# Optimization experiments

Measured on AMD Instinct MI355X. Metric: run time of the kernel, lower is better.

Reference implementation:

```python
import jax, jax.numpy as jnp
import numpy as np

# Production-scale dims
B, DZ, NW, NH, K = 8, 32, 48, 48, 25          # batch, dim_z, grid width/height, n_objects_max
W_RAW = H_RAW = 384.0                          # raw image size
SIZE_MIN, SIZE_MAX = 12.0, 48.0                # object size bounds
SCORE_T, OVER_T = 0.1, 0.3                     # score_threshold, overlap_threshold


def _conv1x1(x, w, b):
    # x: (B, d, nW, nH), w: (o, d), b: (o,) -> (B, o, nW, nH)  [Decoder1by1Linear]
    return jnp.einsum('bdwh,od->bowh', x, w) + b[None, :, None, None]


def _to_box_list(x):
    # (B, nW, nH) -> (N, B) with N = nW*nH, matching convert_to_box_list's permute(2,3,0,1).view
    return jnp.transpose(x, (1, 2, 0)).reshape(-1, x.shape[0])


def _nms(probT, x1, y1, x2, y2, k_max, score_t, over_t):
    # probT, x1..y2: (B, N). Greedy score/overlap NMS -> idx (B, K) int32, mask (B, N) float
    area = (x2 - x1) * (y2 - y1)
    xi1 = jnp.maximum(x1[:, :, None], x1[:, None, :])
    yi1 = jnp.maximum(y1[:, :, None], y1[:, None, :])
    xi2 = jnp.minimum(x2[:, :, None], x2[:, None, :])
    yi2 = jnp.minimum(y2[:, :, None], y2[:, None, :])
    inter = jnp.clip(xi2 - xi1, 0.0) * jnp.clip(yi2 - yi1, 0.0)
    union = area[:, :, None] + area[:, None, :] - inter
    iou = inter / jnp.maximum(union, 1e-8)                      # (B, N, N)
    possible0 = probT > score_t
    Bsz, N = probT.shape
    idx0 = jnp.zeros((Bsz, k_max), jnp.int32)
    val0 = jnp.zeros((Bsz, k_max), bool)

    def body(k, carry):
        possible, idxb, valb = carry
        masked = jnp.where(possible, probT, -jnp.inf)
        sel = jnp.argmax(masked, axis=1).astype(jnp.int32)      # (B,)
        ok = jnp.take_along_axis(possible, sel[:, None], axis=1)[:, 0]
        row = jnp.take_along_axis(iou, sel[:, None, None], axis=1)[:, 0, :]
        possible = possible & (row <= over_t)                   # suppresses sel itself (IoU=1)
        return possible, idxb.at[:, k].set(sel), valb.at[:, k].set(ok)

    _, idxb, valb = jax.lax.fori_loop(0, k_max, body, (possible0, idx0, val0))
    mask = jnp.zeros((Bsz, N), probT.dtype).at[jnp.arange(Bsz)[:, None], idxb].max(
        valb.astype(probT.dtype))
    return idxb, mask


def setup_inputs() -> dict:
    key = jax.random.key(0)
    ks = jax.random.split(key, 5)
    return {
        'zwhere_sample': jax.random.normal(ks[0], (B, DZ, NW, NH), jnp.float32),
        'w_zwhere': 0.2 * jax.random.normal(ks[1], (4, DZ), jnp.float32),
        'b_zwhere': jnp.zeros((4,), jnp.float32),
        'logit_sample': jax.random.normal(ks[2], (B, DZ, NW, NH), jnp.float32),
        'w_logit': 0.2 * jax.random.normal(ks[3], (1, DZ), jnp.float32),
        'b_logit': jnp.zeros((1,), jnp.float32),
        'weight_logits': jax.random.normal(ks[4], (K, B, 1, int(W_RAW), int(H_RAW)), jnp.float32),
    }


def reference(zwhere_sample, w_zwhere, b_zwhere, logit_sample, w_logit, b_logit, weight_logits):
    nW, nH = zwhere_sample.shape[-2:]
    # --- box decoding from zwhere latent map ---
    t = jax.nn.sigmoid(_conv1x1(zwhere_sample, w_zwhere, b_zwhere))  # (B,4,nW,nH)
    tx, ty, tw, th = t[:, 0], t[:, 1], t[:, 2], t[:, 3]
    ix = jnp.arange(nW, dtype=t.dtype)[:, None]   # ij meshgrid rows
    iy = jnp.arange(nH, dtype=t.dtype)[None, :]
    bx = W_RAW * (ix + tx) / nW
    by = H_RAW * (iy + ty) / nH
    bw = SIZE_MIN + (SIZE_MAX - SIZE_MIN) * tw
    bh = SIZE_MIN + (SIZE_MAX - SIZE_MIN) * th
    bx_l, by_l = _to_box_list(bx), _to_box_list(by)   # (N, B)
    bw_l, bh_l = _to_box_list(bw), _to_box_list(bh)
    # --- probability map from logit latent map ---
    p_map = jax.nn.sigmoid(_conv1x1(logit_sample, w_logit, b_logit))  # (B,1,nW,nH)
    prob_all = _to_box_list(p_map[:, 0])              # (N, B)
    probT = prob_all.T                                 # (B, N)
    x1 = (bx_l - 0.5 * bw_l).T
    x2 = (bx_l + 0.5 * bw_l).T
    y1 = (by_l - 0.5 * bh_l).T
    y2 = (by_l + 0.5 * bh_l).T
    # --- NMS under stop_gradient (torch.no_grad in original) ---
    sg = jax.lax.stop_gradient
    idxb, maskB = _nms(sg(probT), sg(x1), sg(y1), sg(x2), sg(y2), K, SCORE_T, OVER_T)
    # prob_few = gather(prob_all * nms_mask, index_top_k): differentiable w.r.t. prob_all
    prob_few = jnp.take_along_axis(probT * maskB, idxb, axis=1).T   # (K, B)
    # --- mask compositing (from_weights_to_masks over the object dim) ---
    big_weight = jax.nn.softplus(weight_logits)       # (K, B, 1, W, H)
    sum_w = jnp.sum(big_weight, axis=0, keepdims=True)
    big_mask = jnp.tanh(sum_w) * (big_weight / jnp.clip(sum_w, 1e-6))
    # probability-weighted masks (downstream compositing)
    return prob_few[:, :, None, None, None] * big_mask  # (K, B, 1, W, H)
```

## Files before the change

kernel.cpp:

```cpp
#include <hip/hip_runtime.h>
#include <math.h>

#define BATCH 8
#define DZ    32
#define NWH   48
#define NBOX  (NWH*NWH)
#define KMAX  25
#define PIX   (384*384)
#define NTOT  (BATCH*NBOX)
#define NW9   9

typedef float vfloat4 __attribute__((ext_vector_type(4)));

__device__ __forceinline__ float sigm(float x) { return 1.0f / (1.0f + expf(-x)); }
__device__ __forceinline__ float sp_fast(float x) {
    return fmaxf(x, 0.0f) + __logf(1.0f + __expf(-fabsf(x)));
}

__global__ __launch_bounds__(64) void conv_kernel(
    const float* __restrict__ z, const float* __restrict__ wz, const float* __restrict__ bz,
    const float* __restrict__ lg, const float* __restrict__ wl, const float* __restrict__ bl,
    float* __restrict__ ws)
{
    int t = blockIdx.x * 64 + threadIdx.x;
    int b = t / 576, j = t % 576;
    int iw = j / 12, ihq = j % 12;

    const float* zb = z  + (((size_t)b * DZ) * NWH + iw) * NWH + ihq * 4;
    const float* lb = lg + (((size_t)b * DZ) * NWH + iw) * NWH + ihq * 4;
    float b0 = bz[0], b1 = bz[1], b2 = bz[2], b3 = bz[3], blg = bl[0];
    vfloat4 a0 = {b0,b0,b0,b0}, a1 = {b1,b1,b1,b1}, a2 = {b2,b2,b2,b2},
            a3 = {b3,b3,b3,b3}, al = {blg,blg,blg,blg};
    #pragma unroll 8
    for (int d = 0; d < DZ; ++d) {
        vfloat4 zv = *(const vfloat4*)(zb + (size_t)d * NBOX);
        vfloat4 lv = *(const vfloat4*)(lb + (size_t)d * NBOX);
        float w0 = wz[d], w1 = wz[32+d], w2 = wz[64+d], w3 = wz[96+d], wv = wl[d];
        a0 += zv * w0; a1 += zv * w1; a2 += zv * w2; a3 += zv * w3; al += lv * wv;
    }

    float t0v[4] = {a0.x,a0.y,a0.z,a0.w};
    float t1v[4] = {a1.x,a1.y,a1.z,a1.w};
    float t2v[4] = {a2.x,a2.y,a2.z,a2.w};
    float t3v[4] = {a3.x,a3.y,a3.z,a3.w};
    float alv[4] = {al.x,al.y,al.z,al.w};
    float x1o[4], y1o[4], x2o[4], y2o[4], po[4];
    #pragma unroll
    for (int c = 0; c < 4; ++c) {
        float tx = sigm(t0v[c]), ty = sigm(t1v[c]), tw = sigm(t2v[c]), th = sigm(t3v[c]);
        float bx = 8.0f * ((float)iw + tx);
        float by = 8.0f * ((float)(ihq*4 + c) + ty);
        float bw = 12.0f + 36.0f * tw;
        float bh = 12.0f + 36.0f * th;
        x1o[c] = bx - 0.5f*bw;  y1o[c] = by - 0.5f*bh;
        x2o[c] = bx + 0.5f*bw;  y2o[c] = by + 0.5f*bh;
        po[c]  = sigm(alv[c]);
    }
    int o = b * NBOX + iw * NWH + ihq * 4;
    *(vfloat4*)(ws + 0*NTOT + o) = (vfloat4){x1o[0],x1o[1],x1o[2],x1o[3]};
    *(vfloat4*)(ws + 1*NTOT + o) = (vfloat4){y1o[0],y1o[1],y1o[2],y1o[3]};
    *(vfloat4*)(ws + 2*NTOT + o) = (vfloat4){x2o[0],x2o[1],x2o[2],x2o[3]};
    *(vfloat4*)(ws + 3*NTOT + o) = (vfloat4){y2o[0],y2o[1],y2o[2],y2o[3]};
    *(vfloat4*)(ws + 4*NTOT + o) = (vfloat4){po[0], po[1], po[2], po[3]};
}

__global__ __launch_bounds__(576) void nms_kernel(const float* __restrict__ ws,
                                                  float* __restrict__ pfT)
{
    __shared__ vfloat4 boxS[NBOX];
    __shared__ float   prS[NBOX];
    __shared__ unsigned long long keyB[2][NW9];
    __shared__ int idxA[KMAX], okA[KMAX];

    const int b = blockIdx.x, t = threadIdx.x;
    const int n0 = t * 4;
    const int o  = b * NBOX + n0;

    vfloat4 X1 = *(const vfloat4*)(ws + 0*NTOT + o);
    vfloat4 Y1 = *(const vfloat4*)(ws + 1*NTOT + o);
    vfloat4 X2 = *(const vfloat4*)(ws + 2*NTOT + o);
    vfloat4 Y2 = *(const vfloat4*)(ws + 3*NTOT + o);
    vfloat4 P  = *(const vfloat4*)(ws + 4*NTOT + o);

    float x1r[4] = {X1.x,X1.y,X1.z,X1.w};
    float y1r[4] = {Y1.x,Y1.y,Y1.z,Y1.w};
    float x2r[4] = {X2.x,X2.y,X2.z,X2.w};
    float y2r[4] = {Y2.x,Y2.y,Y2.z,Y2.w};
    float pv [4] = {P.x, P.y, P.z, P.w};
    float arr[4], mkv[4];
    #pragma unroll
    for (int c = 0; c < 4; ++c) {
        arr[c] = (x2r[c]-x1r[c]) * (y2r[c]-y1r[c]);
        mkv[c] = (pv[c] > 0.1f) ? pv[c] : -INFINITY;
        boxS[n0+c] = (vfloat4){x1r[c], y1r[c], x2r[c], y2r[c]};
        prS [n0+c] = pv[c];
    }
    __syncthreads();

    float sx1=0.f, sy1=0.f, sx2=0.f, sy2=0.f, sar=0.f;
    for (int k = 0; k < KMAX; ++k) {
        unsigned long long best = 0ULL;
        #pragma unroll
        for (int c = 0; c < 4; ++c) {
            if (k > 0 && mkv[c] != -INFINITY) {
                float xi1 = fmaxf(sx1, x1r[c]);
                float yi1 = fmaxf(sy1, y1r[c]);
                float xi2 = fminf(sx2, x2r[c]);
                float yi2 = fminf(sy2, y2r[c]);
                float inter = fmaxf(xi2 - xi1, 0.f) * fmaxf(yi2 - yi1, 0.f);
                float uni   = sar + arr[c] - inter;
                float iou   = inter / fmaxf(uni, 1e-8f);
                if (iou > 0.3f) mkv[c] = -INFINITY;
            }
            if (mkv[c] != -INFINITY) {
                unsigned long long kk =
                    ((unsigned long long)__float_as_uint(mkv[c]) << 32) | (unsigned int)(~(n0+c));
                if (kk > best) best = kk;
            }
        }
        #pragma unroll
        for (int off = 32; off > 0; off >>= 1) {
            unsigned long long o2 = __shfl_down(best, off);
            if (o2 > best) best = o2;
        }
        if ((t & 63) == 0) keyB[k & 1][t >> 6] = best;
        __syncthreads();
        unsigned long long m = keyB[k & 1][0];
        #pragma unroll
        for (int w = 1; w < NW9; ++w) {
            unsigned long long o2 = keyB[k & 1][w];
            if (o2 > m) m = o2;
        }
        int sel = (m == 0ULL) ? 0 : (int)(~(unsigned int)(m & 0xFFFFFFFFULL));
        if (t == 0) { idxA[k] = sel; okA[k] = (m != 0ULL); }
        vfloat4 sb = boxS[sel];
        sx1 = sb.x; sy1 = sb.y; sx2 = sb.z; sy2 = sb.w;
        sar = (sx2 - sx1) * (sy2 - sy1);
    }

    if (t == 0) {
        #pragma unroll 1
        for (int k = 0; k < KMAX; ++k) {
            float mm = 0.f;
            for (int k2 = 0; k2 < KMAX; ++k2)
                if (idxA[k2] == idxA[k] && okA[k2]) mm = 1.f;
            pfT[b * 32 + k] = prS[idxA[k]] * mm;
        }
    }
}

__global__ __launch_bounds__(256) void big_kernel(const float* __restrict__ wlg,
                                                  const float* __restrict__ pfT,
                                                  float* __restrict__ out)
{
    __shared__ vfloat4 accS[4][64];

    const size_t stride = (size_t)BATCH * PIX;
    const int t = threadIdx.x;
    const int w = t >> 6;
    const int l = t & 63;
    const int kb = 6 * w;
    const size_t j = (size_t)blockIdx.x * 256 + (size_t)l * 4;
    const int b = blockIdx.x / 576;
    const float* base = wlg + (size_t)kb * stride + j;

    vfloat4 acc = {0.f, 0.f, 0.f, 0.f};
    vfloat4 sp0, sp1, sp2, sp3, sp4, sp5;
#define LOADSP(s) { vfloat4 v = *(const vfloat4*)(base + (size_t)(s) * stride); \
    sp##s = (vfloat4){ sp_fast(v.x), sp_fast(v.y), sp_fast(v.z), sp_fast(v.w) }; \
    acc += sp##s; }
    LOADSP(0) LOADSP(1) LOADSP(2) LOADSP(3) LOADSP(4) LOADSP(5)
#undef LOADSP
    vfloat4 sp6 = {0.f, 0.f, 0.f, 0.f};
    if (w == 3) {
        vfloat4 v = *(const vfloat4*)(base + (size_t)6 * stride);
        sp6 = (vfloat4){ sp_fast(v.x), sp_fast(v.y), sp_fast(v.z), sp_fast(v.w) };
        acc += sp6;
    }

    accS[w][l] = acc;
    __syncthreads();
    vfloat4 S4 = accS[0][l] + accS[1][l] + accS[2][l] + accS[3][l];

    vfloat4 m;
    {
        float ex = __expf(-2.f*S4.x), ey = __expf(-2.f*S4.y),
              ez = __expf(-2.f*S4.z), ew = __expf(-2.f*S4.w);
        m.x = (1.f - ex) * __builtin_amdgcn_rcpf(1.f + ex) * __builtin_amdgcn_rcpf(fmaxf(S4.x, 1e-6f));
        m.y = (1.f - ey) * __builtin_amdgcn_rcpf(1.f + ey) * __builtin_amdgcn_rcpf(fmaxf(S4.y, 1e-6f));
        m.z = (1.f - ez) * __builtin_amdgcn_rcpf(1.f + ez) * __builtin_amdgcn_rcpf(fmaxf(S4.z, 1e-6f));
        m.w = (1.f - ew) * __builtin_amdgcn_rcpf(1.f + ew) * __builtin_amdgcn_rcpf(fmaxf(S4.w, 1e-6f));
    }

    const float* pfb = pfT + b * 32 + kb;
    float* ob = out + (size_t)kb * stride + j;
#define STORE(s) { float c = pfb[s]; \
    vfloat4 o = { c * m.x * sp##s.x, c * m.y * sp##s.y, c * m.z * sp##s.z, c * m.w * sp##s.w }; \
    *(vfloat4*)(ob + (size_t)(s) * stride) = o; }
    STORE(0) STORE(1) STORE(2) STORE(3) STORE(4) STORE(5)
#undef STORE
    if (w == 3) {
        float c = pfb[6];
        vfloat4 o = { c * m.x * sp6.x, c * m.y * sp6.y, c * m.z * sp6.z, c * m.w * sp6.w };
        *(vfloat4*)(ob + (size_t)6 * stride) = o;
    }
}

extern "C" void kernel_launch(void* const* d_in, const int* in_sizes, int n_in,
                              void* d_out, int out_size, void* d_ws, size_t ws_size,
                              hipStream_t stream)
{
    const float* zwhere = (const float*)d_in[0];
    const float* w_zw   = (const float*)d_in[1];
    const float* b_zw   = (const float*)d_in[2];
    const float* logit  = (const float*)d_in[3];
    const float* w_lg   = (const float*)d_in[4];
    const float* b_lg   = (const float*)d_in[5];
    const float* wlogit = (const float*)d_in[6];
    float* out = (float*)d_out;
    float* ws  = (float*)d_ws;
    float* pfT = ws + 5 * NTOT;

    conv_kernel<<<(BATCH*576)/64, 64, 0, stream>>>(zwhere, w_zw, b_zw, logit, w_lg, b_lg, ws);
    nms_kernel<<<BATCH, 576, 0, stream>>>(ws, pfT);
    big_kernel<<<(BATCH * PIX) / 256, 256, 0, stream>>>(wlogit, pfT, out);
}
```

Measured before the change: 96.76 us.

## Compute full K reduction per thread and stage softplus values in fp16 LDS

The big kernel now has each thread handle all 25 object slices for one 4-pixel vector, instead of splitting the slices across four waves and reducing through shared memory. The softplus values are kept in shared memory as packed fp16 between the sum pass and the output pass, so the per-thread register footprint stays small. Each block covers four times as many pixels. This removes the cross-wave sync and reduction, but it lowers precision of the stored mask weights and uses about 51KB of LDS per block, which may limit occupancy in this memory-bound kernel.

After: 96.21 us. No clear change (-0.6%).

```diff
diff --git a/kernel.cpp b/kernel.cpp
--- a/kernel.cpp
+++ b/kernel.cpp
@@ -1,4 +1,5 @@
 #include <hip/hip_runtime.h>
+#include <hip/hip_fp16.h>
 #include <math.h>
 
 #define BATCH 8
@@ -153,56 +154,50 @@
                                                   const float* __restrict__ pfT,
                                                   float* __restrict__ out)
 {
-    __shared__ vfloat4 accS[4][64];
+    __shared__ uint2 spL[KMAX * 256];
 
     const size_t stride = (size_t)BATCH * PIX;
     const int t = threadIdx.x;
-    const int w = t >> 6;
-    const int l = t & 63;
-    const int kb = 6 * w;
-    const size_t j = (size_t)blockIdx.x * 256 + (size_t)l * 4;
-    const int b = blockIdx.x / 576;
-    const float* base = wlg + (size_t)kb * stride + j;
-
-    vfloat4 acc = {0.f, 0.f, 0.f, 0.f};
-    vfloat4 sp0, sp1, sp2, sp3, sp4, sp5;
-#define LOADSP(s) { vfloat4 v = *(const vfloat4*)(base + (size_t)(s) * stride); \
-    sp##s = (vfloat4){ sp_fast(v.x), sp_fast(v.y), sp_fast(v.z), sp_fast(v.w) }; \
-    acc += sp##s; }
-    LOADSP(0) LOADSP(1) LOADSP(2) LOADSP(3) LOADSP(4) LOADSP(5)
-#undef LOADSP
-    vfloat4 sp6 = {0.f, 0.f, 0.f, 0.f};
-    if (w == 3) {
-        vfloat4 v = *(const vfloat4*)(base + (size_t)6 * stride);
-        sp6 = (vfloat4){ sp_fast(v.x), sp_fast(v.y), sp_fast(v.z), sp_fast(v.w) };
-        acc += sp6;
-    }
-
-    accS[w][l] = acc;
-    __syncthreads();
-    vfloat4 S4 = accS[0][l] + accS[1][l] + accS[2][l] + accS[3][l];
+    const size_t jb = (size_t)blockIdx.x * 1024 + (size_t)t * 4;
+    const int b = blockIdx.x / 144;
+    const float* base = wlg + jb;
+
+    vfloat4 S = {0.f, 0.f, 0.f, 0.f};
+    #pragma unroll
+    for (int k = 0; k < KMAX; ++k) {
+        vfloat4 v = *(const vfloat4*)(base + (size_t)k * stride);
+        float sx = sp_fast(v.x), sy = sp_fast(v.y), sz = sp_fast(v.z), sw = sp_fast(v.w);
+        S.x += sx; S.y += sy; S.z += sz; S.w += sw;
+        __half2 h01 = __floats2half2_rn(sx, sy);
+        __half2 h23 = __floats2half2_rn(sz, sw);
+        uint2 pk;
+        pk.x = *(unsigned int*)&h01;
+        pk.y = *(unsigned int*)&h23;
+        spL[k * 256 + t] = pk;
+    }
 
     vfloat4 m;
     {
-        float ex = __expf(-2.f*S4.x), ey = __expf(-2.f*S4.y),
-              ez = __expf(-2.f*S4.z), ew = __expf(-2.f*S4.w);
-        m.x = (1.f - ex) * __builtin_amdgcn_rcpf(1.f + ex) * __builtin_amdgcn_rcpf(fmaxf(S4.x, 1e-6f));
-        m.y = (1.f - ey) * __builtin_amdgcn_rcpf(1.f + ey) * __builtin_amdgcn_rcpf(fmaxf(S4.y, 1e-6f));
-        m.z = (1.f - ez) * __builtin_amdgcn_rcpf(1.f + ez) * __builtin_amdgcn_rcpf(fmaxf(S4.z, 1e-6f));
-        m.w = (1.f - ew) * __builtin_amdgcn_rcpf(1.f + ew) * __builtin_amdgcn_rcpf(fmaxf(S4.w, 1e-6f));
-    }
-
-    const float* pfb = pfT + b * 32 + kb;
-    float* ob = out + (size_t)kb * stride + j;
-#define STORE(s) { float c = pfb[s]; \
-    vfloat4 o = { c * m.x * sp##s.x, c * m.y * sp##s.y, c * m.z * sp##s.z, c * m.w * sp##s.w }; \
-    *(vfloat4*)(ob + (size_t)(s) * stride) = o; }
-    STORE(0) STORE(1) STORE(2) STORE(3) STORE(4) STORE(5)
-#undef STORE
-    if (w == 3) {
-        float c = pfb[6];
-        vfloat4 o = { c * m.x * sp6.x, c * m.y * sp6.y, c * m.z * sp6.z, c * m.w * sp6.w };
-        *(vfloat4*)(ob + (size_t)6 * stride) = o;
+        float ex = __expf(-2.f*S.x), ey = __expf(-2.f*S.y),
+              ez = __expf(-2.f*S.z), ew = __expf(-2.f*S.w);
+        m.x = (1.f - ex) * __builtin_amdgcn_rcpf(1.f + ex) * __builtin_amdgcn_rcpf(fmaxf(S.x, 1e-6f));
+        m.y = (1.f - ey) * __builtin_amdgcn_rcpf(1.f + ey) * __builtin_amdgcn_rcpf(fmaxf(S.y, 1e-6f));
+        m.z = (1.f - ez) * __builtin_amdgcn_rcpf(1.f + ez) * __builtin_amdgcn_rcpf(fmaxf(S.z, 1e-6f));
+        m.w = (1.f - ew) * __builtin_amdgcn_rcpf(1.f + ew) * __builtin_amdgcn_rcpf(fmaxf(S.w, 1e-6f));
+    }
+
+    const float* pfb = pfT + b * 32;
+    float* ob = out + jb;
+    #pragma unroll
+    for (int k = 0; k < KMAX; ++k) {
+        uint2 pk = spL[k * 256 + t];
+        __half2 h01 = *(__half2*)&pk.x;
+        __half2 h23 = *(__half2*)&pk.y;
+        float2 a = __half22float2(h01);
+        float2 d = __half22float2(h23);
+        float c = pfb[k];
+        vfloat4 o = { c * m.x * a.x, c * m.y * a.y, c * m.z * d.x, c * m.w * d.y };
+        *(vfloat4*)(ob + (size_t)k * stride) = o;
     }
 }
 
@@ -223,5 +218,5 @@
 
     conv_kernel<<<(BATCH*576)/64, 64, 0, stream>>>(zwhere, w_zw, b_zw, logit, w_lg, b_lg, ws);
     nms_kernel<<<BATCH, 576, 0, stream>>>(ws, pfT);
-    big_kernel<<<(BATCH * PIX) / 256, 256, 0, stream>>>(wlogit, pfT, out);
-}
+    big_kernel<<<(BATCH * PIX) / 1024, 256, 0, stream>>>(wlogit, pfT, out);
+}
```
